# Performance work log

Hardware: AMD Instinct MI355X
Metric: run time of the kernel (lower is better)

## Reference

```python
import jax, jax.numpy as jnp
import numpy as np

W_ACTION_COUNT = 1.0
W_ACTION_TENSOR = 2.0


def setup_inputs() -> dict:
    key = jax.random.key(0)
    k1, k2, k3 = jax.random.split(key, 3)
    B, A, F = 4096, 2048, 8  # batch, max_actions, feature dim (axis-1 length = A + 1)
    predictions = jax.random.normal(k1, (B, A + 1, F), dtype=jnp.float32)
    targets = jax.random.normal(k2, (B, A + 1, F), dtype=jnp.float32)
    # Ground-truth action counts are integers stored as floats at [:, 0, 0].
    # Include zeros so the valid-batch filtering path is exercised.
    counts = jax.random.randint(k3, (B,), 0, A + 1).astype(jnp.float32)
    targets = targets.at[:, 0, 0].set(counts)
    return {"predictions": predictions, "targets": targets}


def reference(predictions, targets):
    # predictions/targets: (B, A+1, 8); index 0 along axis 1 carries the action count.
    pred_counts = predictions[:, 0, 0]            # (B,)
    target_counts = targets[:, 0, 0]              # (B,)
    pred_actions = predictions[:, 1:, :]          # (B, A, 8)
    target_actions = targets[:, 1:, :]            # (B, A, 8)

    count_loss = jnp.mean((pred_counts - target_counts) ** 2)

    A = pred_actions.shape[1]
    counts_int = target_counts.astype(jnp.int32)  # int(count.item()) truncation
    valid = counts_int > 0                        # (B,)
    mask = jnp.arange(A, dtype=jnp.int32)[None, :] < counts_int[:, None]  # (B, A)

    sq = (pred_actions - target_actions) ** 2     # (B, A, 8)
    per_sample_sum = jnp.sum(sq * mask[:, :, None].astype(sq.dtype), axis=(1, 2))  # (B,)
    denom = (counts_int * pred_actions.shape[2]).astype(sq.dtype)  # count * 8 elements
    per_sample_mse = jnp.where(valid, per_sample_sum / jnp.maximum(denom, 1.0), 0.0)

    n_valid = jnp.sum(valid.astype(sq.dtype))
    action_tensor_loss = jnp.sum(per_sample_mse) / jnp.maximum(n_valid, 1.0)

    total = W_ACTION_COUNT * count_loss + jnp.where(
        n_valid > 0, W_ACTION_TENSOR * action_tensor_loss, 0.0
    )
    return total
```

## Files before the change

kernel.cpp:

```cpp
#include <hip/hip_runtime.h>

#define AP1   2049
#define FEAT  8
#define ROWF  (AP1 * FEAT)


__global__ void init_ws_kernel(float* ws) {
    if (threadIdx.x < 3) ws[threadIdx.x] = 0.0f;
}

__device__ __forceinline__ float block_reduce_sum(float v) {
    #pragma unroll
    for (int o = 32; o > 0; o >>= 1) v += __shfl_down(v, o, 64);
    __shared__ float sm[4];
    const int wid  = threadIdx.x >> 6;
    const int lane = threadIdx.x & 63;
    if (lane == 0) sm[wid] = v;
    __syncthreads();
    if (wid == 0) {
        v = (lane < 4) ? sm[lane] : 0.0f;
        v += __shfl_down(v, 2, 64);
        v += __shfl_down(v, 1, 64);
    }
    return v;
}

__global__ __launch_bounds__(256) void loss_main_kernel(
        const float* __restrict__ pred,
        const float* __restrict__ targ,
        float* __restrict__ ws) {
    const int b = blockIdx.x;
    const float* pb = pred + (size_t)b * ROWF;
    const float* tb = targ + (size_t)b * ROWF;

    const float tc = tb[0];
    const float pc = pb[0];
    const int count = (int)tc;

    const int nvec = count * 2;
    const float4* p4 = (const float4*)(pb + FEAT);
    const float4* t4 = (const float4*)(tb + FEAT);

    float s = 0.0f;
    for (int i = threadIdx.x; i < nvec; i += blockDim.x) {
        const float4 a = p4[i];
        const float4 c = t4[i];
        const float dx = a.x - c.x;
        const float dy = a.y - c.y;
        const float dz = a.z - c.z;
        const float dw = a.w - c.w;
        s += dx * dx + dy * dy + dz * dz + dw * dw;
    }

    const float total = block_reduce_sum(s);

    if (threadIdx.x == 0) {
        const float d = pc - tc;
        atomicAdd(&ws[0], d * d);
        if (count > 0) {
            atomicAdd(&ws[1], total / (float)(count * FEAT));
            atomicAdd(&ws[2], 1.0f);
        }
    }
}

__global__ void finalize_kernel(const float* __restrict__ ws,
                                float* __restrict__ out, float invB) {
    const float count_loss = ws[0] * invB;
    const float nv = ws[2];
    const float atl = (nv > 0.0f) ? (ws[1] / nv) : 0.0f;
    out[0] = count_loss + 2.0f * atl;
}

extern "C" void kernel_launch(void* const* d_in, const int* in_sizes, int n_in,
                              void* d_out, int out_size, void* d_ws, size_t ws_size,
                              hipStream_t stream) {
    const float* pred = (const float*)d_in[0];
    const float* targ = (const float*)d_in[1];
    float* out = (float*)d_out;
    float* ws  = (float*)d_ws;

    const int B = in_sizes[0] / ROWF;

    init_ws_kernel<<<1, 64, 0, stream>>>(ws);
    loss_main_kernel<<<B, 256, 0, stream>>>(pred, targ, ws);
    finalize_kernel<<<1, 1, 0, stream>>>(ws, out, 1.0f / (float)B);
}
```

Measured before the change: 528.9 us.

## Replace global atomics with per-batch partials and unroll the load loop

Each block now writes its count error, per-sample MSE and valid flag to its own workspace slot. A single-block reduce kernel sums those slots, which removes the init kernel and the atomic contention on three global floats. The main loop is unrolled four times so each thread has more independent float4 loads in flight. Batch size is now hardcoded to 4096 instead of being derived from the input size.

```diff
diff --git a/kernel.cpp b/kernel.cpp
--- a/kernel.cpp
+++ b/kernel.cpp
@@ -1,29 +1,10 @@
 #include <hip/hip_runtime.h>
 
+#define NB    4096
 #define AP1   2049
 #define FEAT  8
 #define ROWF  (AP1 * FEAT)
 
-
-__global__ void init_ws_kernel(float* ws) {
-    if (threadIdx.x < 3) ws[threadIdx.x] = 0.0f;
-}
-
-__device__ __forceinline__ float block_reduce_sum(float v) {
-    #pragma unroll
-    for (int o = 32; o > 0; o >>= 1) v += __shfl_down(v, o, 64);
-    __shared__ float sm[4];
-    const int wid  = threadIdx.x >> 6;
-    const int lane = threadIdx.x & 63;
-    if (lane == 0) sm[wid] = v;
-    __syncthreads();
-    if (wid == 0) {
-        v = (lane < 4) ? sm[lane] : 0.0f;
-        v += __shfl_down(v, 2, 64);
-        v += __shfl_down(v, 1, 64);
-    }
-    return v;
-}
 
 __global__ __launch_bounds__(256) void loss_main_kernel(
         const float* __restrict__ pred,
@@ -42,7 +23,29 @@
     const float4* t4 = (const float4*)(tb + FEAT);
 
     float s = 0.0f;
-    for (int i = threadIdx.x; i < nvec; i += blockDim.x) {
+    int i = (int)threadIdx.x;
+    const int stride = 256;
+
+    for (; i + 3 * stride < nvec; i += 4 * stride) {
+        const float4 a0 = p4[i];
+        const float4 a1 = p4[i + stride];
+        const float4 a2 = p4[i + 2 * stride];
+        const float4 a3 = p4[i + 3 * stride];
+        const float4 c0 = t4[i];
+        const float4 c1 = t4[i + stride];
+        const float4 c2 = t4[i + 2 * stride];
+        const float4 c3 = t4[i + 3 * stride];
+        float dx, dy, dz, dw;
+        dx = a0.x - c0.x; dy = a0.y - c0.y; dz = a0.z - c0.z; dw = a0.w - c0.w;
+        s += dx * dx + dy * dy + dz * dz + dw * dw;
+        dx = a1.x - c1.x; dy = a1.y - c1.y; dz = a1.z - c1.z; dw = a1.w - c1.w;
+        s += dx * dx + dy * dy + dz * dz + dw * dw;
+        dx = a2.x - c2.x; dy = a2.y - c2.y; dz = a2.z - c2.z; dw = a2.w - c2.w;
+        s += dx * dx + dy * dy + dz * dz + dw * dw;
+        dx = a3.x - c3.x; dy = a3.y - c3.y; dz = a3.z - c3.z; dw = a3.w - c3.w;
+        s += dx * dx + dy * dy + dz * dz + dw * dw;
+    }
+    for (; i < nvec; i += stride) {
         const float4 a = p4[i];
         const float4 c = t4[i];
         const float dx = a.x - c.x;
@@ -52,24 +55,51 @@
         s += dx * dx + dy * dy + dz * dz + dw * dw;
     }
 
-    const float total = block_reduce_sum(s);
+    #pragma unroll
+    for (int o = 32; o > 0; o >>= 1) s += __shfl_down(s, o, 64);
+    __shared__ float sm[4];
+    const int wid  = threadIdx.x >> 6;
+    const int lane = threadIdx.x & 63;
+    if (lane == 0) sm[wid] = s;
+    __syncthreads();
 
     if (threadIdx.x == 0) {
+        const float total = sm[0] + sm[1] + sm[2] + sm[3];
         const float d = pc - tc;
-        atomicAdd(&ws[0], d * d);
-        if (count > 0) {
-            atomicAdd(&ws[1], total / (float)(count * FEAT));
-            atomicAdd(&ws[2], 1.0f);
-        }
+        ws[b] = d * d;
+        const bool valid = (count > 0);
+        ws[NB + b]     = valid ? (total / (float)(count * FEAT)) : 0.0f;
+        ws[2 * NB + b] = valid ? 1.0f : 0.0f;
     }
 }
 
-__global__ void finalize_kernel(const float* __restrict__ ws,
-                                float* __restrict__ out, float invB) {
-    const float count_loss = ws[0] * invB;
-    const float nv = ws[2];
-    const float atl = (nv > 0.0f) ? (ws[1] / nv) : 0.0f;
-    out[0] = count_loss + 2.0f * atl;
+__global__ __launch_bounds__(256) void reduce_kernel(
+        const float* __restrict__ ws, float* __restrict__ out) {
+    float s0 = 0.0f, s1 = 0.0f, s2 = 0.0f;
+    for (int i = threadIdx.x; i < NB; i += 256) {
+        s0 += ws[i];
+        s1 += ws[NB + i];
+        s2 += ws[2 * NB + i];
+    }
+    #pragma unroll
+    for (int o = 32; o > 0; o >>= 1) {
+        s0 += __shfl_down(s0, o, 64);
+        s1 += __shfl_down(s1, o, 64);
+        s2 += __shfl_down(s2, o, 64);
+    }
+    __shared__ float sm[3][4];
+    const int wid  = threadIdx.x >> 6;
+    const int lane = threadIdx.x & 63;
+    if (lane == 0) { sm[0][wid] = s0; sm[1][wid] = s1; sm[2][wid] = s2; }
+    __syncthreads();
+    if (threadIdx.x == 0) {
+        const float count_sum = sm[0][0] + sm[0][1] + sm[0][2] + sm[0][3];
+        const float mse_sum   = sm[1][0] + sm[1][1] + sm[1][2] + sm[1][3];
+        const float nv        = sm[2][0] + sm[2][1] + sm[2][2] + sm[2][3];
+        const float count_loss = count_sum * (1.0f / (float)NB);
+        const float atl = (nv > 0.0f) ? (mse_sum / nv) : 0.0f;
+        out[0] = count_loss + 2.0f * atl;
+    }
 }
 
 extern "C" void kernel_launch(void* const* d_in, const int* in_sizes, int n_in,
@@ -80,9 +110,6 @@
     float* out = (float*)d_out;
     float* ws  = (float*)d_ws;
 
-    const int B = in_sizes[0] / ROWF;
-
-    init_ws_kernel<<<1, 64, 0, stream>>>(ws);
-    loss_main_kernel<<<B, 256, 0, stream>>>(pred, targ, ws);
-    finalize_kernel<<<1, 1, 0, stream>>>(ws, out, 1.0f / (float)B);
+    loss_main_kernel<<<NB, 256, 0, stream>>>(pred, targ, ws);
+    reduce_kernel<<<1, 256, 0, stream>>>(ws, out);
 }
```

Result: faster. 465.1 us (-12.1%).

## Load-balance masked MSE via prefix scan of counts and flat row indexing

Applied to the files above, without the earlier changes.

Replaces the one-block-per-sample kernel with four phases: gather the counts, prefix-scan them, then spread every valid action row evenly over a fixed grid, using a binary search on the scan to find each row's sample, and finally reduce. This removes the load imbalance of samples with widely varying counts and the atomics, using deterministic per-block partials instead. In exchange it adds two extra launches, a single-block scan, a 16KB shared copy of the scan per block, and a 12-step binary search per row. Each thread now reads one 32-byte row per step rather than coalescing float4 across contiguous lanes, though adjacent threads still touch adjacent rows.

```diff
diff --git a/kernel.cpp b/kernel.cpp
--- a/kernel.cpp
+++ b/kernel.cpp
@@ -1,75 +1,139 @@
 #include <hip/hip_runtime.h>
 
+#define NB    4096
 #define AP1   2049
 #define FEAT  8
 #define ROWF  (AP1 * FEAT)
+#define G2_BLOCKS 2048
+#define G2_THREADS 256
+#define G0_BLOCKS (NB / 256)
 
+#define WS_RS   0
+#define WS_CNT  4112
+#define WS_P2   (WS_CNT + NB)
+#define WS_P0C  (WS_P2 + G2_BLOCKS)
+#define WS_P0V  (WS_P0C + 16)
 
-__global__ void init_ws_kernel(float* ws) {
-    if (threadIdx.x < 3) ws[threadIdx.x] = 0.0f;
-}
-
-__device__ __forceinline__ float block_reduce_sum(float v) {
+__device__ __forceinline__ float block_reduce_256(float v, float* sm) {
     #pragma unroll
     for (int o = 32; o > 0; o >>= 1) v += __shfl_down(v, o, 64);
-    __shared__ float sm[4];
     const int wid  = threadIdx.x >> 6;
     const int lane = threadIdx.x & 63;
     if (lane == 0) sm[wid] = v;
     __syncthreads();
-    if (wid == 0) {
-        v = (lane < 4) ? sm[lane] : 0.0f;
-        v += __shfl_down(v, 2, 64);
-        v += __shfl_down(v, 1, 64);
-    }
-    return v;
+    return sm[0] + sm[1] + sm[2] + sm[3];
 }
 
-__global__ __launch_bounds__(256) void loss_main_kernel(
-        const float* __restrict__ pred,
-        const float* __restrict__ targ,
-        float* __restrict__ ws) {
-    const int b = blockIdx.x;
-    const float* pb = pred + (size_t)b * ROWF;
-    const float* tb = targ + (size_t)b * ROWF;
+__global__ __launch_bounds__(256) void phase0_gather(
+        const float* __restrict__ pred, const float* __restrict__ targ,
+        int* __restrict__ wsi, float* __restrict__ wsf) {
+    const int b = blockIdx.x * 256 + threadIdx.x;
+    const float tc = targ[(size_t)b * ROWF];
+    const float pc = pred[(size_t)b * ROWF];
+    const int cnt = (int)tc;
+    wsi[WS_CNT + b] = cnt;
+    const float d = pc - tc;
 
-    const float tc = tb[0];
-    const float pc = pb[0];
-    const int count = (int)tc;
-
-    const int nvec = count * 2;
-    const float4* p4 = (const float4*)(pb + FEAT);
-    const float4* t4 = (const float4*)(tb + FEAT);
-
-    float s = 0.0f;
-    for (int i = threadIdx.x; i < nvec; i += blockDim.x) {
-        const float4 a = p4[i];
-        const float4 c = t4[i];
-        const float dx = a.x - c.x;
-        const float dy = a.y - c.y;
-        const float dz = a.z - c.z;
-        const float dw = a.w - c.w;
-        s += dx * dx + dy * dy + dz * dz + dw * dw;
-    }
-
-    const float total = block_reduce_sum(s);
-
+    __shared__ float sm[4];
+    const float closs = block_reduce_256(d * d, sm);
+    __syncthreads();
+    const float nval = block_reduce_256(cnt > 0 ? 1.0f : 0.0f, sm);
     if (threadIdx.x == 0) {
-        const float d = pc - tc;
-        atomicAdd(&ws[0], d * d);
-        if (count > 0) {
-            atomicAdd(&ws[1], total / (float)(count * FEAT));
-            atomicAdd(&ws[2], 1.0f);
-        }
+        wsf[WS_P0C + blockIdx.x] = closs;
+        wsf[WS_P0V + blockIdx.x] = nval;
     }
 }
 
-__global__ void finalize_kernel(const float* __restrict__ ws,
-                                float* __restrict__ out, float invB) {
-    const float count_loss = ws[0] * invB;
-    const float nv = ws[2];
-    const float atl = (nv > 0.0f) ? (ws[1] / nv) : 0.0f;
-    out[0] = count_loss + 2.0f * atl;
+__global__ __launch_bounds__(1024) void phase1_scan(int* __restrict__ wsi) {
+    const int t = threadIdx.x;
+    const int4 c = *(const int4*)&wsi[WS_CNT + 4 * t];
+    const int s_own = c.x + c.y + c.z + c.w;
+
+    __shared__ int sc[1024];
+    sc[t] = s_own;
+    __syncthreads();
+    #pragma unroll
+    for (int off = 1; off < 1024; off <<= 1) {
+        int v = (t >= off) ? sc[t - off] : 0;
+        __syncthreads();
+        sc[t] += v;
+        __syncthreads();
+    }
+    const int excl = sc[t] - s_own;
+
+    int4 rs;
+    rs.x = excl;
+    rs.y = excl + c.x;
+    rs.z = rs.y + c.y;
+    rs.w = rs.z + c.z;
+    *(int4*)&wsi[WS_RS + 4 * t] = rs;
+    if (t == 1023) wsi[WS_RS + NB] = sc[1023];
+}
+
+__global__ __launch_bounds__(G2_THREADS) void phase2_main(
+        const float* __restrict__ pred, const float* __restrict__ targ,
+        const int* __restrict__ wsi, float* __restrict__ wsf) {
+    __shared__ int rs[NB + 1];
+    __shared__ float sm[4];
+    for (int i = threadIdx.x; i <= NB; i += G2_THREADS)
+        rs[i] = wsi[WS_RS + i];
+    __syncthreads();
+
+    const int T = rs[NB];
+    float s = 0.0f;
+    const int stride = G2_BLOCKS * G2_THREADS;
+
+    for (int r = blockIdx.x * G2_THREADS + threadIdx.x; r < T; r += stride) {
+        int lo = 0, hi = NB;
+        #pragma unroll
+        for (int it = 0; it < 12; ++it) {
+            const int mid = (lo + hi) >> 1;
+            if (rs[mid] <= r) lo = mid; else hi = mid;
+        }
+        const int b = lo;
+        const int local = r - rs[b];
+        const int cnt8 = (rs[b + 1] - rs[b]) * FEAT;
+        const size_t base = (size_t)b * ROWF + FEAT + (size_t)local * FEAT;
+
+        const float4 a0 = *(const float4*)(pred + base);
+        const float4 a1 = *(const float4*)(pred + base + 4);
+        const float4 c0 = *(const float4*)(targ + base);
+        const float4 c1 = *(const float4*)(targ + base + 4);
+
+        float dx, dy, dz, dw, sq;
+        dx = a0.x - c0.x; dy = a0.y - c0.y; dz = a0.z - c0.z; dw = a0.w - c0.w;
+        sq = dx * dx + dy * dy + dz * dz + dw * dw;
+        dx = a1.x - c1.x; dy = a1.y - c1.y; dz = a1.z - c1.z; dw = a1.w - c1.w;
+        sq += dx * dx + dy * dy + dz * dz + dw * dw;
+
+        s += sq / (float)cnt8;
+    }
+
+    const float total = block_reduce_256(s, sm);
+    if (threadIdx.x == 0) wsf[WS_P2 + blockIdx.x] = total;
+}
+
+__global__ __launch_bounds__(256) void phase3_final(
+        const float* __restrict__ wsf, float* __restrict__ out) {
+    float s = 0.0f;
+    for (int i = threadIdx.x; i < G2_BLOCKS; i += 256) s += wsf[WS_P2 + i];
+    float cl = 0.0f, nv = 0.0f;
+    if (threadIdx.x < 16) {
+        cl = wsf[WS_P0C + threadIdx.x];
+        nv = wsf[WS_P0V + threadIdx.x];
+    }
+    __shared__ float sm[4];
+    const float mse_sum = block_reduce_256(s, sm);
+    __syncthreads();
+    const float count_sum = block_reduce_256(cl, sm);
+    __syncthreads();
+    const float n_valid = block_reduce_256(nv, sm);
+
+    if (threadIdx.x == 0) {
+        const float count_loss = count_sum * (1.0f / (float)NB);
+        const float atl = (n_valid > 0.0f) ? (mse_sum / n_valid) : 0.0f;
+        out[0] = count_loss + 2.0f * atl;
+    }
 }
 
 extern "C" void kernel_launch(void* const* d_in, const int* in_sizes, int n_in,
@@ -78,11 +142,11 @@
     const float* pred = (const float*)d_in[0];
     const float* targ = (const float*)d_in[1];
     float* out = (float*)d_out;
-    float* ws  = (float*)d_ws;
+    int*   wsi = (int*)d_ws;
+    float* wsf = (float*)d_ws;
 
-    const int B = in_sizes[0] / ROWF;
-
-    init_ws_kernel<<<1, 64, 0, stream>>>(ws);
-    loss_main_kernel<<<B, 256, 0, stream>>>(pred, targ, ws);
-    finalize_kernel<<<1, 1, 0, stream>>>(ws, out, 1.0f / (float)B);
+    phase0_gather<<<G0_BLOCKS, 256, 0, stream>>>(pred, targ, wsi, wsf);
+    phase1_scan<<<1, 1024, 0, stream>>>(wsi);
+    phase2_main<<<G2_BLOCKS, G2_THREADS, 0, stream>>>(pred, targ, wsi, wsf);
+    phase3_final<<<1, 256, 0, stream>>>(wsf, out);
 }
```

Measured after the change: 467.9 us. 11.5% less time.
